# Performance work log

Measured on AMD Instinct MI355X. Metric: run time of the kernel, lower is better.

## Reference

```python
import jax, jax.numpy as jnp
import numpy as np

B, D, LC, LQ = 64, 128, 1024, 128
NEG = -1e30


def setup_inputs() -> dict:
    key = jax.random.key(0)
    k1, k2, k3 = jax.random.split(key, 3)
    lim = float(np.sqrt(1.0 / D))
    return {
        "C": jax.random.normal(k1, (B, D, LC), dtype=jnp.float32),
        "Q": jax.random.normal(k2, (B, D, LQ), dtype=jnp.float32),
        "cmask": jnp.ones((B, LC), dtype=jnp.float32),
        "qmask": jnp.ones((B, LQ), dtype=jnp.float32),
        "w": jax.random.uniform(k3, (3 * D,), dtype=jnp.float32, minval=-lim, maxval=lim),
    }


def reference(C, Q, cmask, qmask, w):
    # C: [B, D, Lc], Q: [B, D, Lq] -> transpose to [B, L, D] as in the torch module
    Ct = jnp.swapaxes(C, 1, 2)  # [B, Lc, D]
    Qt = jnp.swapaxes(Q, 1, 2)  # [B, Lq, D]
    d = Ct.shape[-1]
    # Trilinear decomposition of the per-step concat([Qi, C, Q*C]) . w loop:
    # S[b,c,q] = Qt[b,q] . w_q + Ct[b,c] . w_c + (Ct[b,c] * w_m) . Qt[b,q]
    w_q, w_c, w_m = w[:d], w[d:2 * d], w[2 * d:]
    s_q = Qt @ w_q                                   # [B, Lq]
    s_c = Ct @ w_c                                   # [B, Lc]
    s_m = jnp.einsum("bcd,bqd->bcq", Ct * w_m, Qt)   # [B, Lc, Lq]
    S = s_m + s_c[:, :, None] + s_q[:, None, :]      # [B, Lc, Lq]

    S1 = jax.nn.softmax(S + (1.0 - qmask)[:, None, :] * NEG, axis=2)
    S2 = jax.nn.softmax(S + (1.0 - cmask)[:, :, None] * NEG, axis=1)

    A = jnp.einsum("bcq,bqd->bcd", S1, Qt)           # [B, Lc, D]
    S12 = jnp.einsum("bcq,bkq->bck", S1, S2)         # [B, Lc, Lc]
    Bt = jnp.einsum("bck,bkd->bcd", S12, Ct)         # [B, Lc, D]

    out = jnp.concatenate([Ct, A, Ct * A, Ct * Bt], axis=2)  # [B, Lc, 4D]
    # dropout is identity in eval mode
    return jnp.swapaxes(out, 1, 2)                   # [B, 4D, Lc]
```

## Files before the change

### kernel.cpp

```cpp
#include <hip/hip_runtime.h>
#include <cstdint>
#include <cstddef>

#define B_  64
#define D_  128
#define LC_ 1024
#define LQ_ 128
#define NEGV (-1e30f)
#define NINF (-3.402823466e38f)

typedef short s16x8 __attribute__((ext_vector_type(8)));
typedef float f32x4 __attribute__((ext_vector_type(4)));

__device__ __forceinline__ unsigned short f2bf(float x) {
    union { float f; unsigned u; } v; v.f = x;
    unsigned r = v.u + 0x7fffu + ((v.u >> 16) & 1u);
    return (unsigned short)(r >> 16);
}
__device__ __forceinline__ float bf2f(unsigned short x) {
    union { unsigned u; float f; } v; v.u = ((unsigned)x) << 16;
    return v.f;
}

__global__ __launch_bounds__(256) void kT_C(const float* __restrict__ C,
                                            const float* __restrict__ w,
                                            unsigned short* __restrict__ CWt,
                                            unsigned short* __restrict__ Cb,
                                            float* __restrict__ sc_g) {
    __shared__ float tile[32][33];
    __shared__ float wc_l[128], wm_l[128];
    __shared__ float red[8][32];
    int t = threadIdx.x;
    int b = blockIdx.y, c0 = blockIdx.x * 32;
    if (t < 128) { wc_l[t] = w[D_ + t]; wm_l[t] = w[2 * D_ + t]; }
    __syncthreads();
    float scp = 0.f;
    int cc = t & 31, db = t >> 5;
    for (int ch = 0; ch < 4; ch++) {
#pragma unroll
        for (int i = 0; i < 4; i++) {
            int dl = db * 4 + i;
            float v = C[((size_t)(b * D_ + ch * 32 + dl)) * LC_ + c0 + cc];
            tile[dl][cc] = v;
            scp += v * wc_l[ch * 32 + dl];
        }
        __syncthreads();
        {
            int c2 = t >> 3, ds = (t & 7) * 4;
            ushort4 o;
            o.x = f2bf(tile[ds + 0][c2] * wm_l[ch * 32 + ds + 0]);
            o.y = f2bf(tile[ds + 1][c2] * wm_l[ch * 32 + ds + 1]);
            o.z = f2bf(tile[ds + 2][c2] * wm_l[ch * 32 + ds + 2]);
            o.w = f2bf(tile[ds + 3][c2] * wm_l[ch * 32 + ds + 3]);
            *(ushort4*)&CWt[((size_t)(b * LC_ + c0 + c2)) * D_ + ch * 32 + ds] = o;
        }
        {
            int d2 = t >> 3, cs = (t & 7) * 4;
            ushort4 o;
            o.x = f2bf(tile[d2][cs + 0]);
            o.y = f2bf(tile[d2][cs + 1]);
            o.z = f2bf(tile[d2][cs + 2]);
            o.w = f2bf(tile[d2][cs + 3]);
            *(ushort4*)&Cb[((size_t)(b * D_ + ch * 32 + d2)) * LC_ + c0 + cs] = o;
        }
        __syncthreads();
    }
    red[db][cc] = scp;
    __syncthreads();
    if (t < 32) {
        float s = 0.f;
#pragma unroll
        for (int j = 0; j < 8; j++) s += red[j][t];
        sc_g[b * LC_ + c0 + t] = s;
    }
}

__global__ __launch_bounds__(256) void kT_Q(const float* __restrict__ Q,
                                            const float* __restrict__ w,
                                            unsigned short* __restrict__ Qt,
                                            unsigned short* __restrict__ Qb,
                                            float* __restrict__ sq_g) {
    __shared__ float tile[32][33];
    __shared__ float wq_l[128];
    __shared__ float red[8][32];
    int t = threadIdx.x;
    int b = blockIdx.y, q0 = blockIdx.x * 32;
    if (t < 128) wq_l[t] = w[t];
    __syncthreads();
    float sqp = 0.f;
    int qq = t & 31, db = t >> 5;
    for (int ch = 0; ch < 4; ch++) {
#pragma unroll
        for (int i = 0; i < 4; i++) {
            int dl = db * 4 + i;
            float v = Q[((size_t)(b * D_ + ch * 32 + dl)) * LQ_ + q0 + qq];
            tile[dl][qq] = v;
            sqp += v * wq_l[ch * 32 + dl];
        }
        __syncthreads();
        {
            int q2 = t >> 3, ds = (t & 7) * 4;
            ushort4 o;
            o.x = f2bf(tile[ds + 0][q2]);
            o.y = f2bf(tile[ds + 1][q2]);
            o.z = f2bf(tile[ds + 2][q2]);
            o.w = f2bf(tile[ds + 3][q2]);
            *(ushort4*)&Qt[((size_t)(b * LQ_ + q0 + q2)) * D_ + ch * 32 + ds] = o;
        }
        {
            int d2 = t >> 3, qs = (t & 7) * 4;
            ushort4 o;
            o.x = f2bf(tile[d2][qs + 0]);
            o.y = f2bf(tile[d2][qs + 1]);
            o.z = f2bf(tile[d2][qs + 2]);
            o.w = f2bf(tile[d2][qs + 3]);
            *(ushort4*)&Qb[((size_t)(b * D_ + ch * 32 + d2)) * LQ_ + q0 + qs] = o;
        }
        __syncthreads();
    }
    red[db][qq] = sqp;
    __syncthreads();
    if (t < 32) {
        float s = 0.f;
#pragma unroll
        for (int j = 0; j < 8; j++) s += red[j][t];
        sq_g[b * LQ_ + q0 + t] = s;
    }
}

__global__ __launch_bounds__(256) void kA_S(const unsigned short* __restrict__ CWt,
                                            const unsigned short* __restrict__ Qt,
                                            const float* __restrict__ sc_g,
                                            const float* __restrict__ sq_g,
                                            const float* __restrict__ cmask,
                                            const float* __restrict__ qmask,
                                            unsigned short* __restrict__ S1b,
                                            float* __restrict__ g_g,
                                            float* __restrict__ pmax_g,
                                            float* __restrict__ psum_g) {
    __shared__ unsigned short S1t[128 * 136];
    __shared__ float sc_l[128], sq_l[128], cmv_l[128], qmv_l[128];
    int t = threadIdx.x;
    int b = blockIdx.y, c0 = blockIdx.x * 128;
    if (t < 128) {
        sc_l[t] = sc_g[b * LC_ + c0 + t];
        sq_l[t] = sq_g[b * LQ_ + t];
        cmv_l[t] = (1.0f - cmask[b * LC_ + c0 + t]) * NEGV;
        qmv_l[t] = (1.0f - qmask[b * LQ_ + t]) * NEGV;
    }
    __syncthreads();
    int wv = t >> 6, l = t & 63, quad = l >> 4, lp = l & 15;
    int w32 = wv * 32;
    f32x4 zero = {0.f, 0.f, 0.f, 0.f};
    f32x4 acc[2][8];
#pragma unroll
    for (int mc = 0; mc < 2; mc++)
#pragma unroll
        for (int qt = 0; qt < 8; qt++) acc[mc][qt] = zero;

#pragma unroll
    for (int ks = 0; ks < 4; ks++) {
        s16x8 a[2], bb[8];
        a[0] = *(const s16x8*)&CWt[((size_t)(b * LC_ + c0 + w32 + lp)) * D_ + ks * 32 + quad * 8];
        a[1] = *(const s16x8*)&CWt[((size_t)(b * LC_ + c0 + w32 + 16 + lp)) * D_ + ks * 32 + quad * 8];
#pragma unroll
        for (int qt = 0; qt < 8; qt++)
            bb[qt] = *(const s16x8*)&Qt[((size_t)(b * LQ_ + qt * 16 + lp)) * D_ + ks * 32 + quad * 8];
#pragma unroll
        for (int mc = 0; mc < 2; mc++)
#pragma unroll
            for (int qt = 0; qt < 8; qt++)
                acc[mc][qt] = __builtin_amdgcn_mfma_f32_16x16x32_bf16(a[mc], bb[qt], acc[mc][qt], 0, 0, 0);
    }
#pragma unroll
    for (int mc = 0; mc < 2; mc++)
#pragma unroll
        for (int qt = 0; qt < 8; qt++)
#pragma unroll
            for (int i = 0; i < 4; i++)
                acc[mc][qt][i] += sc_l[w32 + mc * 16 + quad * 4 + i] + sq_l[qt * 16 + lp];

    float qmv_r[8];
#pragma unroll
    for (int qt = 0; qt < 8; qt++) qmv_r[qt] = qmv_l[qt * 16 + lp];

    float rm_r[2][4], ri_r[2][4];
#pragma unroll
    for (int mc = 0; mc < 2; mc++)
#pragma unroll
        for (int i = 0; i < 4; i++) {
            float m = NINF;
#pragma unroll
            for (int qt = 0; qt < 8; qt++) m = fmaxf(m, acc[mc][qt][i] + qmv_r[qt]);
#pragma unroll
            for (int off = 1; off < 16; off <<= 1) m = fmaxf(m, __shfl_xor(m, off, 64));
            float s = 0.f;
#pragma unroll
            for (int qt = 0; qt < 8; qt++) s += __expf(acc[mc][qt][i] + qmv_r[qt] - m);
#pragma unroll
            for (int off = 1; off < 16; off <<= 1) s += __shfl_xor(s, off, 64);
            rm_r[mc][i] = m;
            ri_r[mc][i] = 1.0f / s;
            int row = w32 + mc * 16 + quad * 4 + i;
            if (lp == 0) g_g[b * LC_ + c0 + row] = s * __expf(m + cmv_l[row]);
        }

    float cmv_r[2][4];
#pragma unroll
    for (int mc = 0; mc < 2; mc++)
#pragma unroll
        for (int i = 0; i < 4; i++) cmv_r[mc][i] = cmv_l[w32 + mc * 16 + quad * 4 + i];
    int chunk = blockIdx.x * 4 + wv;
#pragma unroll
    for (int qt = 0; qt < 8; qt++) {
        float cm = NINF;
#pragma unroll
        for (int mc = 0; mc < 2; mc++)
#pragma unroll
            for (int i = 0; i < 4; i++) cm = fmaxf(cm, acc[mc][qt][i] + cmv_r[mc][i]);
        cm = fmaxf(cm, __shfl_xor(cm, 16, 64));
        cm = fmaxf(cm, __shfl_xor(cm, 32, 64));
        float cs = 0.f;
#pragma unroll
        for (int mc = 0; mc < 2; mc++)
#pragma unroll
            for (int i = 0; i < 4; i++) cs += __expf(acc[mc][qt][i] + cmv_r[mc][i] - cm);
        cs += __shfl_xor(cs, 16, 64);
        cs += __shfl_xor(cs, 32, 64);
        if (l < 16) {
            pmax_g[((size_t)(b * 32 + chunk)) * LQ_ + qt * 16 + lp] = cm;
            psum_g[((size_t)(b * 32 + chunk)) * LQ_ + qt * 16 + lp] = cs;
        }
    }

#pragma unroll
    for (int mc = 0; mc < 2; mc++)
#pragma unroll
        for (int qt = 0; qt < 8; qt++)
#pragma unroll
            for (int i = 0; i < 4; i++) {
                int row = w32 + mc * 16 + quad * 4 + i;
                float s1 = __expf(acc[mc][qt][i] + qmv_r[qt] - rm_r[mc][i]) * ri_r[mc][i];
                S1t[row * 136 + qt * 16 + lp] = f2bf(s1);
            }
    __syncthreads();
    {
        int row = t >> 1, qh = (t & 1) * 64;
        const uint4* src = (const uint4*)&S1t[row * 136 + qh];
        uint4* dst = (uint4*)&S1b[((size_t)(b * LC_ + c0 + row)) * LQ_ + qh];
#pragma unroll
        for (int j = 0; j < 8; j++) dst[j] = src[j];
    }
}

__global__ __launch_bounds__(128) void k2b(const float* __restrict__ pmax,
                                           const float* __restrict__ psum,
                                           float* __restrict__ hq_g,
                                           float* __restrict__ ci_g) {
    int q = threadIdx.x, b = blockIdx.x;
    float m = NINF;
    for (int j = 0; j < 32; j++) m = fmaxf(m, pmax[((size_t)(b * 32 + j)) * LQ_ + q]);
    float s = 0.f;
    for (int j = 0; j < 32; j++)
        s += psum[((size_t)(b * 32 + j)) * LQ_ + q] * __expf(pmax[((size_t)(b * 32 + j)) * LQ_ + q] - m);
    hq_g[b * LQ_ + q] = __expf(-m);
    ci_g[b * LQ_ + q] = 1.0f / s;
}

__global__ __launch_bounds__(256) void kB_T2(const unsigned short* __restrict__ Cb,
                                             const unsigned short* __restrict__ S1b,
                                             const float* __restrict__ g_g,
                                             const float* __restrict__ hq_g,
                                             float* __restrict__ T2p) {
    __shared__ unsigned short Ew[64 * 72];
    __shared__ float h_l[64];
    int t = threadIdx.x;
    int b = blockIdx.y;
    int kc = blockIdx.x >> 1, nq = blockIdx.x & 1;
    int q0 = nq * 64, cbase = kc * 256;
    if (t < 64) h_l[t] = hq_g[b * LQ_ + q0 + t];
    int wv = t >> 6, l = t & 63, quad = l >> 4, lp = l & 15;
    int w32 = wv * 32;
    f32x4 zero = {0.f, 0.f, 0.f, 0.f};
    f32x4 acc[2][4];
#pragma unroll
    for (int mc = 0; mc < 2; mc++)
#pragma unroll
        for (int nt = 0; nt < 4; nt++) acc[mc][nt] = zero;
    __syncthreads();

    for (int sub = 0; sub < 4; sub++) {
        int csub = cbase + sub * 64;
#pragma unroll
        for (int r = 0; r < 2; r++) {
            int cr = (t >> 3) + 32 * r;
            int qof = (t & 7) * 8;
            float gv = g_g[b * LC_ + csub + cr];
            uint4 v = *(const uint4*)&S1b[((size_t)(b * LC_ + csub + cr)) * LQ_ + q0 + qof];
            const unsigned short* pu = (const unsigned short*)&v;
#pragma unroll
            for (int j = 0; j < 8; j++)
                Ew[(qof + j) * 72 + cr] = f2bf(bf2f(pu[j]) * gv * h_l[qof + j]);
        }
        __syncthreads();
#pragma unroll
        for (int ks = 0; ks < 2; ks++) {
            s16x8 a[2], bb[4];
            a[0] = *(const s16x8*)&Cb[((size_t)(b * D_ + w32 + lp)) * LC_ + csub + ks * 32 + quad * 8];
            a[1] = *(const s16x8*)&Cb[((size_t)(b * D_ + w32 + 16 + lp)) * LC_ + csub + ks * 32 + quad * 8];
#pragma unroll
            for (int nt = 0; nt < 4; nt++)
                bb[nt] = *(const s16x8*)&Ew[(nt * 16 + lp) * 72 + ks * 32 + quad * 8];
#pragma unroll
            for (int mc = 0; mc < 2; mc++)
#pragma unroll
                for (int nt = 0; nt < 4; nt++)
                    acc[mc][nt] = __builtin_amdgcn_mfma_f32_16x16x32_bf16(a[mc], bb[nt], acc[mc][nt], 0, 0, 0);
        }
        __syncthreads();
    }
#pragma unroll
    for (int mc = 0; mc < 2; mc++)
#pragma unroll
        for (int i = 0; i < 4; i++) {
            int d = w32 + mc * 16 + quad * 4 + i;
#pragma unroll
            for (int nt = 0; nt < 4; nt++)
                T2p[(((size_t)kc * B_ + b) * D_ + d) * LQ_ + q0 + nt * 16 + lp] = acc[mc][nt][i];
        }
}

__global__ __launch_bounds__(256) void k3b(const float* __restrict__ T2p,
                                           const float* __restrict__ ci_g,
                                           unsigned short* __restrict__ T2b) {
    int idx = blockIdx.x * 256 + threadIdx.x;
    const size_t N = (size_t)B_ * D_ * LQ_;
    int b = idx >> 14, q = idx & 127;
    float s = T2p[idx] + T2p[idx + N] + T2p[idx + 2 * N] + T2p[idx + 3 * N];
    T2b[idx] = f2bf(s * ci_g[b * LQ_ + q]);
}

__global__ __launch_bounds__(256) void kC_out(const float* __restrict__ C,
                                              const unsigned short* __restrict__ Qb,
                                              const unsigned short* __restrict__ T2b,
                                              const unsigned short* __restrict__ S1b,
                                              float* __restrict__ out) {
    int t = threadIdx.x;
    int b = blockIdx.y, c0 = blockIdx.x * 128;
    int wv = t >> 6, l = t & 63, quad = l >> 4, lp = l & 15;
    int w32 = wv * 32;
    f32x4 zero = {0.f, 0.f, 0.f, 0.f};
    f32x4 accA[2][8], accB[2][8];
#pragma unroll
    for (int mc = 0; mc < 2; mc++)
#pragma unroll
        for (int nt = 0; nt < 8; nt++) { accA[mc][nt] = zero; accB[mc][nt] = zero; }

#pragma unroll
    for (int ks = 0; ks < 4; ks++) {
        s16x8 aq[2], at[2], bb[8];
        aq[0] = *(const s16x8*)&Qb[((size_t)(b * D_ + w32 + lp)) * LQ_ + ks * 32 + quad * 8];
        aq[1] = *(const s16x8*)&Qb[((size_t)(b * D_ + w32 + 16 + lp)) * LQ_ + ks * 32 + quad * 8];
        at[0] = *(const s16x8*)&T2b[((size_t)(b * D_ + w32 + lp)) * LQ_ + ks * 32 + quad * 8];
        at[1] = *(const s16x8*)&T2b[((size_t)(b * D_ + w32 + 16 + lp)) * LQ_ + ks * 32 + quad * 8];
#pragma unroll
        for (int nt = 0; nt < 8; nt++)
            bb[nt] = *(const s16x8*)&S1b[((size_t)(b * LC_ + c0 + nt * 16 + lp)) * LQ_ + ks * 32 + quad * 8];
#pragma unroll
        for (int mc = 0; mc < 2; mc++)
#pragma unroll
            for (int nt = 0; nt < 8; nt++) {
                accA[mc][nt] = __builtin_amdgcn_mfma_f32_16x16x32_bf16(aq[mc], bb[nt], accA[mc][nt], 0, 0, 0);
                accB[mc][nt] = __builtin_amdgcn_mfma_f32_16x16x32_bf16(at[mc], bb[nt], accB[mc][nt], 0, 0, 0);
            }
    }
    const size_t DL = (size_t)D_ * LC_;
#pragma unroll
    for (int mc = 0; mc < 2; mc++)
#pragma unroll
        for (int i = 0; i < 4; i++) {
            int d = w32 + mc * 16 + quad * 4 + i;
            const float* Crow = C + ((size_t)(b * D_ + d)) * LC_ + c0;
            size_t ob = ((size_t)(b * 4 * D_ + d)) * LC_ + c0;
#pragma unroll
            for (int nt = 0; nt < 8; nt++) {
                int c = nt * 16 + lp;
                float cv = Crow[c];
                float a = accA[mc][nt][i];
                float bt = accB[mc][nt][i];
                out[ob + c] = cv;
                out[ob + DL + c] = a;
                out[ob + 2 * DL + c] = cv * a;
                out[ob + 3 * DL + c] = cv * bt;
            }
        }
}

extern "C" void kernel_launch(void* const* d_in, const int* in_sizes, int n_in,
                              void* d_out, int out_size, void* d_ws, size_t ws_size,
                              hipStream_t stream) {
    const float* C     = (const float*)d_in[0];
    const float* Q     = (const float*)d_in[1];
    const float* cmask = (const float*)d_in[2];
    const float* qmask = (const float*)d_in[3];
    const float* w     = (const float*)d_in[4];
    float* out = (float*)d_out;

    unsigned short* us = (unsigned short*)d_ws;
    unsigned short* S1b = us;
    unsigned short* CWt = S1b + (size_t)B_ * LC_ * LQ_;
    unsigned short* Cb  = CWt + (size_t)B_ * LC_ * D_;
    unsigned short* Qt  = Cb  + (size_t)B_ * D_ * LC_;
    unsigned short* Qb  = Qt  + (size_t)B_ * LQ_ * D_;
    unsigned short* T2b = Qb  + (size_t)B_ * D_ * LQ_;
    float* fp = (float*)(T2b + (size_t)B_ * D_ * LQ_);
    float* T2p    = fp;
    float* sc_g   = T2p + (size_t)4 * B_ * D_ * LQ_;
    float* g_g    = sc_g + (size_t)B_ * LC_;
    float* pmax_g = g_g + (size_t)B_ * LC_;
    float* psum_g = pmax_g + (size_t)B_ * 32 * LQ_;
    float* sq_g   = psum_g + (size_t)B_ * 32 * LQ_;
    float* hq_g   = sq_g + (size_t)B_ * LQ_;
    float* ci_g   = hq_g + (size_t)B_ * LQ_;

    kT_C<<<dim3(LC_ / 32, B_), 256, 0, stream>>>(C, w, CWt, Cb, sc_g);
    kT_Q<<<dim3(LQ_ / 32, B_), 256, 0, stream>>>(Q, w, Qt, Qb, sq_g);
    kA_S<<<dim3(LC_ / 128, B_), 256, 0, stream>>>(CWt, Qt, sc_g, sq_g, cmask, qmask,
                                                  S1b, g_g, pmax_g, psum_g);
    k2b<<<dim3(B_), 128, 0, stream>>>(pmax_g, psum_g, hq_g, ci_g);
    kB_T2<<<dim3(8, B_), 256, 0, stream>>>(Cb, S1b, g_g, hq_g, T2p);
    k3b<<<dim3(B_ * D_ * LQ_ / 256), 256, 0, stream>>>(T2p, ci_g, T2b);
    kC_out<<<dim3(LC_ / 128, B_), 256, 0, stream>>>(C, Qb, T2b, S1b, out);
}
```

Before: 254.8 us.

## Emit pre-scaled transposed S1 from score kernel and stage output writes via LDS

The score kernel now also writes a transposed, g-scaled bf16 copy of S1 (q-major) so the T2 GEMM kernel can load MFMA operands directly from global memory, with no LDS staging, per-element rescaling or barriers. The per-column hq scale moves into the final reduction kernel, and the T2 partial split goes from 4 to 8 chunks. The output kernel transposes accumulators through a swizzled LDS tile so it can write float4-coalesced rows instead of scattered scalar stores. The cost is an extra global S1Et buffer, more partial-sum traffic, and an additional bf16 rounding of the g-scaled S1 before the hq factor is applied.

```diff
diff --git a/kernel.cpp b/kernel.cpp
--- a/kernel.cpp
+++ b/kernel.cpp
@@ -21,6 +21,8 @@
     union { unsigned u; float f; } v; v.u = ((unsigned)x) << 16;
     return v.f;
 }
+
+#define SW(r, c) ((c) ^ (((r) & 7) << 2))
 
 __global__ __launch_bounds__(256) void kT_C(const float* __restrict__ C,
                                             const float* __restrict__ w,
@@ -135,11 +137,11 @@
                                             const float* __restrict__ cmask,
                                             const float* __restrict__ qmask,
                                             unsigned short* __restrict__ S1b,
-                                            float* __restrict__ g_g,
+                                            unsigned short* __restrict__ S1Et,
                                             float* __restrict__ pmax_g,
                                             float* __restrict__ psum_g) {
-    __shared__ unsigned short S1t[128 * 136];
-    __shared__ float sc_l[128], sq_l[128], cmv_l[128], qmv_l[128];
+    __shared__ unsigned short Tt[128 * 136];
+    __shared__ float sc_l[128], sq_l[128], cmv_l[128], qmv_l[128], gs[128];
     int t = threadIdx.x;
     int b = blockIdx.y, c0 = blockIdx.x * 128;
     if (t < 128) {
@@ -202,7 +204,7 @@
             rm_r[mc][i] = m;
             ri_r[mc][i] = 1.0f / s;
             int row = w32 + mc * 16 + quad * 4 + i;
-            if (lp == 0) g_g[b * LC_ + c0 + row] = s * __expf(m + cmv_l[row]);
+            if (lp == 0) gs[row] = s * __expf(m + cmv_l[row]);
         }
 
     float cmv_r[2][4];
@@ -241,15 +243,33 @@
             for (int i = 0; i < 4; i++) {
                 int row = w32 + mc * 16 + quad * 4 + i;
                 float s1 = __expf(acc[mc][qt][i] + qmv_r[qt] - rm_r[mc][i]) * ri_r[mc][i];
-                S1t[row * 136 + qt * 16 + lp] = f2bf(s1);
+                Tt[row * 136 + qt * 16 + lp] = f2bf(s1);
             }
     __syncthreads();
     {
         int row = t >> 1, qh = (t & 1) * 64;
-        const uint4* src = (const uint4*)&S1t[row * 136 + qh];
+        const uint4* src = (const uint4*)&Tt[row * 136 + qh];
         uint4* dst = (uint4*)&S1b[((size_t)(b * LC_ + c0 + row)) * LQ_ + qh];
 #pragma unroll
         for (int j = 0; j < 8; j++) dst[j] = src[j];
+    }
+    {
+        int r4 = t >> 2;
+        int cq = (t & 3) * 8;
+#pragma unroll
+        for (int qh = 0; qh < 2; qh++) {
+            int q = qh * 64 + r4;
+#pragma unroll
+            for (int j = 0; j < 4; j++) {
+                int c = j * 32 + cq;
+                uint4 pk;
+                unsigned short* po = (unsigned short*)&pk;
+#pragma unroll
+                for (int k = 0; k < 8; k++)
+                    po[k] = f2bf(bf2f(Tt[(c + k) * 136 + q]) * gs[c + k]);
+                *(uint4*)&S1Et[((size_t)(b * LQ_ + q)) * LC_ + c0 + c] = pk;
+            }
+        }
     }
 }
 
@@ -268,56 +288,33 @@
 }
 
 __global__ __launch_bounds__(256) void kB_T2(const unsigned short* __restrict__ Cb,
-                                             const unsigned short* __restrict__ S1b,
-                                             const float* __restrict__ g_g,
-                                             const float* __restrict__ hq_g,
+                                             const unsigned short* __restrict__ S1Et,
                                              float* __restrict__ T2p) {
-    __shared__ unsigned short Ew[64 * 72];
-    __shared__ float h_l[64];
     int t = threadIdx.x;
-    int b = blockIdx.y;
-    int kc = blockIdx.x >> 1, nq = blockIdx.x & 1;
-    int q0 = nq * 64, cbase = kc * 256;
-    if (t < 64) h_l[t] = hq_g[b * LQ_ + q0 + t];
+    int b = blockIdx.y, kc = blockIdx.x;
+    int cbase = kc * 128;
     int wv = t >> 6, l = t & 63, quad = l >> 4, lp = l & 15;
     int w32 = wv * 32;
     f32x4 zero = {0.f, 0.f, 0.f, 0.f};
-    f32x4 acc[2][4];
-#pragma unroll
-    for (int mc = 0; mc < 2; mc++)
-#pragma unroll
-        for (int nt = 0; nt < 4; nt++) acc[mc][nt] = zero;
-    __syncthreads();
-
-    for (int sub = 0; sub < 4; sub++) {
-        int csub = cbase + sub * 64;
-#pragma unroll
-        for (int r = 0; r < 2; r++) {
-            int cr = (t >> 3) + 32 * r;
-            int qof = (t & 7) * 8;
-            float gv = g_g[b * LC_ + csub + cr];
-            uint4 v = *(const uint4*)&S1b[((size_t)(b * LC_ + csub + cr)) * LQ_ + q0 + qof];
-            const unsigned short* pu = (const unsigned short*)&v;
-#pragma unroll
-            for (int j = 0; j < 8; j++)
-                Ew[(qof + j) * 72 + cr] = f2bf(bf2f(pu[j]) * gv * h_l[qof + j]);
-        }
-        __syncthreads();
-#pragma unroll
-        for (int ks = 0; ks < 2; ks++) {
-            s16x8 a[2], bb[4];
-            a[0] = *(const s16x8*)&Cb[((size_t)(b * D_ + w32 + lp)) * LC_ + csub + ks * 32 + quad * 8];
-            a[1] = *(const s16x8*)&Cb[((size_t)(b * D_ + w32 + 16 + lp)) * LC_ + csub + ks * 32 + quad * 8];
-#pragma unroll
-            for (int nt = 0; nt < 4; nt++)
-                bb[nt] = *(const s16x8*)&Ew[(nt * 16 + lp) * 72 + ks * 32 + quad * 8];
-#pragma unroll
-            for (int mc = 0; mc < 2; mc++)
-#pragma unroll
-                for (int nt = 0; nt < 4; nt++)
-                    acc[mc][nt] = __builtin_amdgcn_mfma_f32_16x16x32_bf16(a[mc], bb[nt], acc[mc][nt], 0, 0, 0);
-        }
-        __syncthreads();
+    f32x4 acc[2][8];
+#pragma unroll
+    for (int mc = 0; mc < 2; mc++)
+#pragma unroll
+        for (int nt = 0; nt < 8; nt++) acc[mc][nt] = zero;
+
+#pragma unroll
+    for (int ks = 0; ks < 4; ks++) {
+        s16x8 a[2], bb[8];
+        a[0] = *(const s16x8*)&Cb[((size_t)(b * D_ + w32 + lp)) * LC_ + cbase + ks * 32 + quad * 8];
+        a[1] = *(const s16x8*)&Cb[((size_t)(b * D_ + w32 + 16 + lp)) * LC_ + cbase + ks * 32 + quad * 8];
+#pragma unroll
+        for (int nt = 0; nt < 8; nt++)
+            bb[nt] = *(const s16x8*)&S1Et[((size_t)(b * LQ_ + nt * 16 + lp)) * LC_ + cbase + ks * 32 + quad * 8];
+#pragma unroll
+        for (int mc = 0; mc < 2; mc++)
+#pragma unroll
+            for (int nt = 0; nt < 8; nt++)
+                acc[mc][nt] = __builtin_amdgcn_mfma_f32_16x16x32_bf16(a[mc], bb[nt], acc[mc][nt], 0, 0, 0);
     }
 #pragma unroll
     for (int mc = 0; mc < 2; mc++)
@@ -325,19 +322,22 @@
         for (int i = 0; i < 4; i++) {
             int d = w32 + mc * 16 + quad * 4 + i;
 #pragma unroll
-            for (int nt = 0; nt < 4; nt++)
-                T2p[(((size_t)kc * B_ + b) * D_ + d) * LQ_ + q0 + nt * 16 + lp] = acc[mc][nt][i];
+            for (int nt = 0; nt < 8; nt++)
+                T2p[(((size_t)kc * B_ + b) * D_ + d) * LQ_ + nt * 16 + lp] = acc[mc][nt][i];
         }
 }
 
 __global__ __launch_bounds__(256) void k3b(const float* __restrict__ T2p,
+                                           const float* __restrict__ hq_g,
                                            const float* __restrict__ ci_g,
                                            unsigned short* __restrict__ T2b) {
     int idx = blockIdx.x * 256 + threadIdx.x;
     const size_t N = (size_t)B_ * D_ * LQ_;
     int b = idx >> 14, q = idx & 127;
-    float s = T2p[idx] + T2p[idx + N] + T2p[idx + 2 * N] + T2p[idx + 3 * N];
-    T2b[idx] = f2bf(s * ci_g[b * LQ_ + q]);
+    float s = 0.f;
+#pragma unroll
+    for (int j = 0; j < 8; j++) s += T2p[idx + j * N];
+    T2b[idx] = f2bf(s * hq_g[b * LQ_ + q] * ci_g[b * LQ_ + q]);
 }
 
 __global__ __launch_bounds__(256) void kC_out(const float* __restrict__ C,
@@ -345,6 +345,7 @@
                                               const unsigned short* __restrict__ T2b,
                                               const unsigned short* __restrict__ S1b,
                                               float* __restrict__ out) {
+    __shared__ float Tile[64 * 132];
     int t = threadIdx.x;
     int b = blockIdx.y, c0 = blockIdx.x * 128;
     int wv = t >> 6, l = t & 63, quad = l >> 4, lp = l & 15;
@@ -374,26 +375,54 @@
                 accB[mc][nt] = __builtin_amdgcn_mfma_f32_16x16x32_bf16(at[mc], bb[nt], accB[mc][nt], 0, 0, 0);
             }
     }
+
     const size_t DL = (size_t)D_ * LC_;
-#pragma unroll
-    for (int mc = 0; mc < 2; mc++)
-#pragma unroll
-        for (int i = 0; i < 4; i++) {
-            int d = w32 + mc * 16 + quad * 4 + i;
-            const float* Crow = C + ((size_t)(b * D_ + d)) * LC_ + c0;
-            size_t ob = ((size_t)(b * 4 * D_ + d)) * LC_ + c0;
-#pragma unroll
-            for (int nt = 0; nt < 8; nt++) {
-                int c = nt * 16 + lp;
-                float cv = Crow[c];
-                float a = accA[mc][nt][i];
-                float bt = accB[mc][nt][i];
-                out[ob + c] = cv;
-                out[ob + DL + c] = a;
-                out[ob + 2 * DL + c] = cv * a;
-                out[ob + 3 * DL + c] = cv * bt;
+    int r = t >> 2;
+    int rw = wv * 16;
+#pragma unroll
+    for (int mc = 0; mc < 2; mc++) {
+        int d_st = (r >> 4) * 32 + mc * 16 + (r & 15);
+        const float* Crow = C + ((size_t)(b * D_ + d_st)) * LC_ + c0;
+        size_t ob = ((size_t)(b * 4 * D_ + d_st)) * LC_ + c0;
+        __syncthreads();
+#pragma unroll
+        for (int nt = 0; nt < 8; nt++)
+#pragma unroll
+            for (int i = 0; i < 4; i++) {
+                int row = rw + quad * 4 + i;
+                Tile[row * 132 + SW(row, nt * 16 + lp)] = accA[mc][nt][i];
             }
-        }
+        __syncthreads();
+#pragma unroll
+        for (int j = 0; j < 8; j++) {
+            int c = j * 16 + (t & 3) * 4;
+            float4 a4 = *(const float4*)&Tile[r * 132 + SW(r, c)];
+            float4 cv = *(const float4*)&Crow[c];
+            *(float4*)&out[ob + c] = cv;
+            *(float4*)&out[ob + DL + c] = a4;
+            float4 ca;
+            ca.x = cv.x * a4.x; ca.y = cv.y * a4.y; ca.z = cv.z * a4.z; ca.w = cv.w * a4.w;
+            *(float4*)&out[ob + 2 * DL + c] = ca;
+        }
+        __syncthreads();
+#pragma unroll
+        for (int nt = 0; nt < 8; nt++)
+#pragma unroll
+            for (int i = 0; i < 4; i++) {
+                int row = rw + quad * 4 + i;
+                Tile[row * 132 + SW(row, nt * 16 + lp)] = accB[mc][nt][i];
+            }
+        __syncthreads();
+#pragma unroll
+        for (int j = 0; j < 8; j++) {
+            int c = j * 16 + (t & 3) * 4;
+            float4 b4 = *(const float4*)&Tile[r * 132 + SW(r, c)];
+            float4 cv = *(const float4*)&Crow[c];
+            float4 cb;
+            cb.x = cv.x * b4.x; cb.y = cv.y * b4.y; cb.z = cv.z * b4.z; cb.w = cv.w * b4.w;
+            *(float4*)&out[ob + 3 * DL + c] = cb;
+        }
+    }
 }
 
 extern "C" void kernel_launch(void* const* d_in, const int* in_sizes, int n_in,
@@ -407,17 +436,17 @@
     float* out = (float*)d_out;
 
     unsigned short* us = (unsigned short*)d_ws;
-    unsigned short* S1b = us;
-    unsigned short* CWt = S1b + (size_t)B_ * LC_ * LQ_;
-    unsigned short* Cb  = CWt + (size_t)B_ * LC_ * D_;
-    unsigned short* Qt  = Cb  + (size_t)B_ * D_ * LC_;
-    unsigned short* Qb  = Qt  + (size_t)B_ * LQ_ * D_;
-    unsigned short* T2b = Qb  + (size_t)B_ * D_ * LQ_;
+    unsigned short* S1b  = us;
+    unsigned short* S1Et = S1b  + (size_t)B_ * LC_ * LQ_;
+    unsigned short* CWt  = S1Et + (size_t)B_ * LQ_ * LC_;
+    unsigned short* Cb   = CWt  + (size_t)B_ * LC_ * D_;
+    unsigned short* Qt   = Cb   + (size_t)B_ * D_ * LC_;
+    unsigned short* Qb   = Qt   + (size_t)B_ * LQ_ * D_;
+    unsigned short* T2b  = Qb   + (size_t)B_ * D_ * LQ_;
     float* fp = (float*)(T2b + (size_t)B_ * D_ * LQ_);
     float* T2p    = fp;
-    float* sc_g   = T2p + (size_t)4 * B_ * D_ * LQ_;
-    float* g_g    = sc_g + (size_t)B_ * LC_;
-    float* pmax_g = g_g + (size_t)B_ * LC_;
+    float* sc_g   = T2p + (size_t)8 * B_ * D_ * LQ_;
+    float* pmax_g = sc_g + (size_t)B_ * LC_;
     float* psum_g = pmax_g + (size_t)B_ * 32 * LQ_;
     float* sq_g   = psum_g + (size_t)B_ * 32 * LQ_;
     float* hq_g   = sq_g + (size_t)B_ * LQ_;
@@ -426,9 +455,9 @@
     kT_C<<<dim3(LC_ / 32, B_), 256, 0, stream>>>(C, w, CWt, Cb, sc_g);
     kT_Q<<<dim3(LQ_ / 32, B_), 256, 0, stream>>>(Q, w, Qt, Qb, sq_g);
     kA_S<<<dim3(LC_ / 128, B_), 256, 0, stream>>>(CWt, Qt, sc_g, sq_g, cmask, qmask,
-                                                  S1b, g_g, pmax_g, psum_g);
+                                                  S1b, S1Et, pmax_g, psum_g);
     k2b<<<dim3(B_), 128, 0, stream>>>(pmax_g, psum_g, hq_g, ci_g);
-    kB_T2<<<dim3(8, B_), 256, 0, stream>>>(Cb, S1b, g_g, hq_g, T2p);
-    k3b<<<dim3(B_ * D_ * LQ_ / 256), 256, 0, stream>>>(T2p, ci_g, T2b);
+    kB_T2<<<dim3(8, B_), 256, 0, stream>>>(Cb, S1Et, T2p);
+    k3b<<<dim3(B_ * D_ * LQ_ / 256), 256, 0, stream>>>(T2p, hq_g, ci_g, T2b);
     kC_out<<<dim3(LC_ / 128, B_), 256, 0, stream>>>(C, Qb, T2b, S1b, out);
 }
```

Measured after the change: 280.6 us. 10.1% more time.

## Fuse C transpose and T2 partial GEMM into score kernel, drop C staging buffers

Applied to the files above, without the earlier changes.

Removes the separate C transpose/convert kernel and the T2 GEMM kernel. The score kernel now loads C directly, builds the w_m-scaled bf16 tile in LDS, computes s_c on the fly, and right after the softmax computes the per-block partial T2 = C·(S1·g) using an LDS-transposed, g-weighted copy of S1. The hq scaling moves into the reduction kernel, which now sums 8 partials instead of 4. The output kernel is retiled to 64 columns to launch more blocks. This avoids writing and re-reading the CWt/Cb/g intermediates and saves two launches, at the cost of more LDS per block, a longer serial kernel, and twice the partial-sum traffic.

```diff
diff --git a/kernel.cpp b/kernel.cpp
--- a/kernel.cpp
+++ b/kernel.cpp
@@ -17,69 +17,12 @@
     unsigned r = v.u + 0x7fffu + ((v.u >> 16) & 1u);
     return (unsigned short)(r >> 16);
 }
-__device__ __forceinline__ float bf2f(unsigned short x) {
-    union { unsigned u; float f; } v; v.u = ((unsigned)x) << 16;
-    return v.f;
-}
-
-__global__ __launch_bounds__(256) void kT_C(const float* __restrict__ C,
-                                            const float* __restrict__ w,
-                                            unsigned short* __restrict__ CWt,
-                                            unsigned short* __restrict__ Cb,
-                                            float* __restrict__ sc_g) {
-    __shared__ float tile[32][33];
-    __shared__ float wc_l[128], wm_l[128];
-    __shared__ float red[8][32];
-    int t = threadIdx.x;
-    int b = blockIdx.y, c0 = blockIdx.x * 32;
-    if (t < 128) { wc_l[t] = w[D_ + t]; wm_l[t] = w[2 * D_ + t]; }
-    __syncthreads();
-    float scp = 0.f;
-    int cc = t & 31, db = t >> 5;
-    for (int ch = 0; ch < 4; ch++) {
-#pragma unroll
-        for (int i = 0; i < 4; i++) {
-            int dl = db * 4 + i;
-            float v = C[((size_t)(b * D_ + ch * 32 + dl)) * LC_ + c0 + cc];
-            tile[dl][cc] = v;
-            scp += v * wc_l[ch * 32 + dl];
-        }
-        __syncthreads();
-        {
-            int c2 = t >> 3, ds = (t & 7) * 4;
-            ushort4 o;
-            o.x = f2bf(tile[ds + 0][c2] * wm_l[ch * 32 + ds + 0]);
-            o.y = f2bf(tile[ds + 1][c2] * wm_l[ch * 32 + ds + 1]);
-            o.z = f2bf(tile[ds + 2][c2] * wm_l[ch * 32 + ds + 2]);
-            o.w = f2bf(tile[ds + 3][c2] * wm_l[ch * 32 + ds + 3]);
-            *(ushort4*)&CWt[((size_t)(b * LC_ + c0 + c2)) * D_ + ch * 32 + ds] = o;
-        }
-        {
-            int d2 = t >> 3, cs = (t & 7) * 4;
-            ushort4 o;
-            o.x = f2bf(tile[d2][cs + 0]);
-            o.y = f2bf(tile[d2][cs + 1]);
-            o.z = f2bf(tile[d2][cs + 2]);
-            o.w = f2bf(tile[d2][cs + 3]);
-            *(ushort4*)&Cb[((size_t)(b * D_ + ch * 32 + d2)) * LC_ + c0 + cs] = o;
-        }
-        __syncthreads();
-    }
-    red[db][cc] = scp;
-    __syncthreads();
-    if (t < 32) {
-        float s = 0.f;
-#pragma unroll
-        for (int j = 0; j < 8; j++) s += red[j][t];
-        sc_g[b * LC_ + c0 + t] = s;
-    }
-}
-
-__global__ __launch_bounds__(256) void kT_Q(const float* __restrict__ Q,
-                                            const float* __restrict__ w,
-                                            unsigned short* __restrict__ Qt,
-                                            unsigned short* __restrict__ Qb,
-                                            float* __restrict__ sq_g) {
+
+__global__ __launch_bounds__(256) void kQ(const float* __restrict__ Q,
+                                          const float* __restrict__ w,
+                                          unsigned short* __restrict__ Qt,
+                                          unsigned short* __restrict__ Qb,
+                                          float* __restrict__ sq_g) {
     __shared__ float tile[32][33];
     __shared__ float wq_l[128];
     __shared__ float red[8][32];
@@ -128,27 +71,67 @@
     }
 }
 
-__global__ __launch_bounds__(256) void kA_S(const unsigned short* __restrict__ CWt,
-                                            const unsigned short* __restrict__ Qt,
-                                            const float* __restrict__ sc_g,
-                                            const float* __restrict__ sq_g,
-                                            const float* __restrict__ cmask,
-                                            const float* __restrict__ qmask,
-                                            unsigned short* __restrict__ S1b,
-                                            float* __restrict__ g_g,
-                                            float* __restrict__ pmax_g,
-                                            float* __restrict__ psum_g) {
-    __shared__ unsigned short S1t[128 * 136];
-    __shared__ float sc_l[128], sq_l[128], cmv_l[128], qmv_l[128];
+__global__ __launch_bounds__(256) void kS(const float* __restrict__ C,
+                                          const unsigned short* __restrict__ Qt,
+                                          const float* __restrict__ w,
+                                          const float* __restrict__ sq_g,
+                                          const float* __restrict__ cmask,
+                                          const float* __restrict__ qmask,
+                                          unsigned short* __restrict__ S1b,
+                                          float* __restrict__ pmax_g,
+                                          float* __restrict__ psum_g,
+                                          float* __restrict__ T2p) {
+    __shared__ unsigned short CW[128 * 136];
+    __shared__ unsigned short Tg[128 * 136];
+    __shared__ float stage[32][33];
+    __shared__ float wc_l[128], wm_l[128], sq_l[128], cmv_l[128], qmv_l[128], sc_l[128];
+    __shared__ float red[8][32];
+
     int t = threadIdx.x;
     int b = blockIdx.y, c0 = blockIdx.x * 128;
     if (t < 128) {
-        sc_l[t] = sc_g[b * LC_ + c0 + t];
+        wc_l[t] = w[D_ + t];
+        wm_l[t] = w[2 * D_ + t];
         sq_l[t] = sq_g[b * LQ_ + t];
         cmv_l[t] = (1.0f - cmask[b * LC_ + c0 + t]) * NEGV;
         qmv_l[t] = (1.0f - qmask[b * LQ_ + t]) * NEGV;
     }
     __syncthreads();
+
+    int cc = t & 31, db = t >> 5;
+    for (int ch = 0; ch < 4; ch++) {
+        float scp = 0.f;
+        for (int dh = 0; dh < 4; dh++) {
+#pragma unroll
+            for (int i = 0; i < 4; i++) {
+                int dl = db * 4 + i;
+                float v = C[((size_t)(b * D_ + dh * 32 + dl)) * LC_ + c0 + ch * 32 + cc];
+                stage[dl][cc] = v;
+                scp += v * wc_l[dh * 32 + dl];
+            }
+            __syncthreads();
+            {
+                int c2 = t >> 3, ds = (t & 7) * 4;
+                ushort4 o;
+                o.x = f2bf(stage[ds + 0][c2] * wm_l[dh * 32 + ds + 0]);
+                o.y = f2bf(stage[ds + 1][c2] * wm_l[dh * 32 + ds + 1]);
+                o.z = f2bf(stage[ds + 2][c2] * wm_l[dh * 32 + ds + 2]);
+                o.w = f2bf(stage[ds + 3][c2] * wm_l[dh * 32 + ds + 3]);
+                *(ushort4*)&CW[(ch * 32 + c2) * 136 + dh * 32 + ds] = o;
+            }
+            __syncthreads();
+        }
+        red[db][cc] = scp;
+        __syncthreads();
+        if (db == 0) {
+            float s = 0.f;
+#pragma unroll
+            for (int j = 0; j < 8; j++) s += red[j][cc];
+            sc_l[ch * 32 + cc] = s;
+        }
+        __syncthreads();
+    }
+
     int wv = t >> 6, l = t & 63, quad = l >> 4, lp = l & 15;
     int w32 = wv * 32;
     f32x4 zero = {0.f, 0.f, 0.f, 0.f};
@@ -161,8 +144,8 @@
 #pragma unroll
     for (int ks = 0; ks < 4; ks++) {
         s16x8 a[2], bb[8];
-        a[0] = *(const s16x8*)&CWt[((size_t)(b * LC_ + c0 + w32 + lp)) * D_ + ks * 32 + quad * 8];
-        a[1] = *(const s16x8*)&CWt[((size_t)(b * LC_ + c0 + w32 + 16 + lp)) * D_ + ks * 32 + quad * 8];
+        a[0] = *(const s16x8*)&CW[(w32 + lp) * 136 + ks * 32 + quad * 8];
+        a[1] = *(const s16x8*)&CW[(w32 + 16 + lp) * 136 + ks * 32 + quad * 8];
 #pragma unroll
         for (int qt = 0; qt < 8; qt++)
             bb[qt] = *(const s16x8*)&Qt[((size_t)(b * LQ_ + qt * 16 + lp)) * D_ + ks * 32 + quad * 8];
@@ -184,11 +167,12 @@
 #pragma unroll
     for (int qt = 0; qt < 8; qt++) qmv_r[qt] = qmv_l[qt * 16 + lp];
 
-    float rm_r[2][4], ri_r[2][4];
+    float rm_r[2][4], ri_r[2][4], gs_r[2][4];
 #pragma unroll
     for (int mc = 0; mc < 2; mc++)
 #pragma unroll
         for (int i = 0; i < 4; i++) {
+            int row = w32 + mc * 16 + quad * 4 + i;
             float m = NINF;
 #pragma unroll
             for (int qt = 0; qt < 8; qt++) m = fmaxf(m, acc[mc][qt][i] + qmv_r[qt]);
@@ -201,8 +185,7 @@
             for (int off = 1; off < 16; off <<= 1) s += __shfl_xor(s, off, 64);
             rm_r[mc][i] = m;
             ri_r[mc][i] = 1.0f / s;
-            int row = w32 + mc * 16 + quad * 4 + i;
-            if (lp == 0) g_g[b * LC_ + c0 + row] = s * __expf(m + cmv_l[row]);
+            gs_r[mc][i] = s * __expf(m + cmv_l[row]);
         }
 
     float cmv_r[2][4];
@@ -233,6 +216,7 @@
         }
     }
 
+    __syncthreads();
 #pragma unroll
     for (int mc = 0; mc < 2; mc++)
 #pragma unroll
@@ -240,17 +224,57 @@
 #pragma unroll
             for (int i = 0; i < 4; i++) {
                 int row = w32 + mc * 16 + quad * 4 + i;
+                int q = qt * 16 + lp;
                 float s1 = __expf(acc[mc][qt][i] + qmv_r[qt] - rm_r[mc][i]) * ri_r[mc][i];
-                S1t[row * 136 + qt * 16 + lp] = f2bf(s1);
-            }
-    __syncthreads();
+                CW[row * 136 + q] = f2bf(s1);
+                Tg[q * 136 + row] = f2bf(s1 * gs_r[mc][i]);
+            }
+    __syncthreads();
+
     {
         int row = t >> 1, qh = (t & 1) * 64;
-        const uint4* src = (const uint4*)&S1t[row * 136 + qh];
+        const uint4* src = (const uint4*)&CW[row * 136 + qh];
         uint4* dst = (uint4*)&S1b[((size_t)(b * LC_ + c0 + row)) * LQ_ + qh];
 #pragma unroll
         for (int j = 0; j < 8; j++) dst[j] = src[j];
     }
+
+    f32x4 acc2[2][8];
+#pragma unroll
+    for (int mc = 0; mc < 2; mc++)
+#pragma unroll
+        for (int nt = 0; nt < 8; nt++) acc2[mc][nt] = zero;
+#pragma unroll
+    for (int ks = 0; ks < 4; ks++) {
+        s16x8 a2[2], bb[8];
+#pragma unroll
+        for (int m = 0; m < 2; m++) {
+            int d = w32 + m * 16 + lp;
+            const float4* p = (const float4*)&C[((size_t)(b * D_ + d)) * LC_ + c0 + ks * 32 + quad * 8];
+            float4 v0 = p[0], v1 = p[1];
+            unsigned short* pp = (unsigned short*)&a2[m];
+            pp[0] = f2bf(v0.x); pp[1] = f2bf(v0.y); pp[2] = f2bf(v0.z); pp[3] = f2bf(v0.w);
+            pp[4] = f2bf(v1.x); pp[5] = f2bf(v1.y); pp[6] = f2bf(v1.z); pp[7] = f2bf(v1.w);
+        }
+#pragma unroll
+        for (int nt = 0; nt < 8; nt++)
+            bb[nt] = *(const s16x8*)&Tg[(nt * 16 + lp) * 136 + ks * 32 + quad * 8];
+#pragma unroll
+        for (int m = 0; m < 2; m++)
+#pragma unroll
+            for (int nt = 0; nt < 8; nt++)
+                acc2[m][nt] = __builtin_amdgcn_mfma_f32_16x16x32_bf16(a2[m], bb[nt], acc2[m][nt], 0, 0, 0);
+    }
+    size_t base = ((size_t)(blockIdx.x * B_ + b)) * ((size_t)D_ * LQ_);
+#pragma unroll
+    for (int mc = 0; mc < 2; mc++)
+#pragma unroll
+        for (int i = 0; i < 4; i++) {
+            int d = w32 + mc * 16 + quad * 4 + i;
+#pragma unroll
+            for (int nt = 0; nt < 8; nt++)
+                T2p[base + (size_t)d * LQ_ + nt * 16 + lp] = acc2[mc][nt][i];
+        }
 }
 
 __global__ __launch_bounds__(128) void k2b(const float* __restrict__ pmax,
@@ -267,77 +291,17 @@
     ci_g[b * LQ_ + q] = 1.0f / s;
 }
 
-__global__ __launch_bounds__(256) void kB_T2(const unsigned short* __restrict__ Cb,
-                                             const unsigned short* __restrict__ S1b,
-                                             const float* __restrict__ g_g,
-                                             const float* __restrict__ hq_g,
-                                             float* __restrict__ T2p) {
-    __shared__ unsigned short Ew[64 * 72];
-    __shared__ float h_l[64];
-    int t = threadIdx.x;
-    int b = blockIdx.y;
-    int kc = blockIdx.x >> 1, nq = blockIdx.x & 1;
-    int q0 = nq * 64, cbase = kc * 256;
-    if (t < 64) h_l[t] = hq_g[b * LQ_ + q0 + t];
-    int wv = t >> 6, l = t & 63, quad = l >> 4, lp = l & 15;
-    int w32 = wv * 32;
-    f32x4 zero = {0.f, 0.f, 0.f, 0.f};
-    f32x4 acc[2][4];
-#pragma unroll
-    for (int mc = 0; mc < 2; mc++)
-#pragma unroll
-        for (int nt = 0; nt < 4; nt++) acc[mc][nt] = zero;
-    __syncthreads();
-
-    for (int sub = 0; sub < 4; sub++) {
-        int csub = cbase + sub * 64;
-#pragma unroll
-        for (int r = 0; r < 2; r++) {
-            int cr = (t >> 3) + 32 * r;
-            int qof = (t & 7) * 8;
-            float gv = g_g[b * LC_ + csub + cr];
-            uint4 v = *(const uint4*)&S1b[((size_t)(b * LC_ + csub + cr)) * LQ_ + q0 + qof];
-            const unsigned short* pu = (const unsigned short*)&v;
-#pragma unroll
-            for (int j = 0; j < 8; j++)
-                Ew[(qof + j) * 72 + cr] = f2bf(bf2f(pu[j]) * gv * h_l[qof + j]);
-        }
-        __syncthreads();
-#pragma unroll
-        for (int ks = 0; ks < 2; ks++) {
-            s16x8 a[2], bb[4];
-            a[0] = *(const s16x8*)&Cb[((size_t)(b * D_ + w32 + lp)) * LC_ + csub + ks * 32 + quad * 8];
-            a[1] = *(const s16x8*)&Cb[((size_t)(b * D_ + w32 + 16 + lp)) * LC_ + csub + ks * 32 + quad * 8];
-#pragma unroll
-            for (int nt = 0; nt < 4; nt++)
-                bb[nt] = *(const s16x8*)&Ew[(nt * 16 + lp) * 72 + ks * 32 + quad * 8];
-#pragma unroll
-            for (int mc = 0; mc < 2; mc++)
-#pragma unroll
-                for (int nt = 0; nt < 4; nt++)
-                    acc[mc][nt] = __builtin_amdgcn_mfma_f32_16x16x32_bf16(a[mc], bb[nt], acc[mc][nt], 0, 0, 0);
-        }
-        __syncthreads();
-    }
-#pragma unroll
-    for (int mc = 0; mc < 2; mc++)
-#pragma unroll
-        for (int i = 0; i < 4; i++) {
-            int d = w32 + mc * 16 + quad * 4 + i;
-#pragma unroll
-            for (int nt = 0; nt < 4; nt++)
-                T2p[(((size_t)kc * B_ + b) * D_ + d) * LQ_ + q0 + nt * 16 + lp] = acc[mc][nt][i];
-        }
-}
-
 __global__ __launch_bounds__(256) void k3b(const float* __restrict__ T2p,
+                                           const float* __restrict__ hq_g,
                                            const float* __restrict__ ci_g,
                                            unsigned short* __restrict__ T2b) {
     int idx = blockIdx.x * 256 + threadIdx.x;
     const size_t N = (size_t)B_ * D_ * LQ_;
     int b = idx >> 14, q = idx & 127;
-    float s = T2p[idx] + T2p[idx + N] + T2p[idx + 2 * N] + T2p[idx + 3 * N];
-    T2b[idx] = f2bf(s * ci_g[b * LQ_ + q]);
+    float s = 0.f;
+#pragma unroll
+    for (int j = 0; j < 8; j++) s += T2p[(size_t)j * N + idx];
+    T2b[idx] = f2bf(s * hq_g[b * LQ_ + q] * ci_g[b * LQ_ + q]);
 }
 
 __global__ __launch_bounds__(256) void kC_out(const float* __restrict__ C,
@@ -346,30 +310,30 @@
                                               const unsigned short* __restrict__ S1b,
                                               float* __restrict__ out) {
     int t = threadIdx.x;
-    int b = blockIdx.y, c0 = blockIdx.x * 128;
+    int b = blockIdx.y, c0 = blockIdx.x * 64;
     int wv = t >> 6, l = t & 63, quad = l >> 4, lp = l & 15;
     int w32 = wv * 32;
     f32x4 zero = {0.f, 0.f, 0.f, 0.f};
-    f32x4 accA[2][8], accB[2][8];
-#pragma unroll
-    for (int mc = 0; mc < 2; mc++)
-#pragma unroll
-        for (int nt = 0; nt < 8; nt++) { accA[mc][nt] = zero; accB[mc][nt] = zero; }
+    f32x4 accA[2][4], accB[2][4];
+#pragma unroll
+    for (int mc = 0; mc < 2; mc++)
+#pragma unroll
+        for (int nt = 0; nt < 4; nt++) { accA[mc][nt] = zero; accB[mc][nt] = zero; }
 
 #pragma unroll
     for (int ks = 0; ks < 4; ks++) {
-        s16x8 aq[2], at[2], bb[8];
+        s16x8 aq[2], at[2], bb[4];
         aq[0] = *(const s16x8*)&Qb[((size_t)(b * D_ + w32 + lp)) * LQ_ + ks * 32 + quad * 8];
         aq[1] = *(const s16x8*)&Qb[((size_t)(b * D_ + w32 + 16 + lp)) * LQ_ + ks * 32 + quad * 8];
         at[0] = *(const s16x8*)&T2b[((size_t)(b * D_ + w32 + lp)) * LQ_ + ks * 32 + quad * 8];
         at[1] = *(const s16x8*)&T2b[((size_t)(b * D_ + w32 + 16 + lp)) * LQ_ + ks * 32 + quad * 8];
 #pragma unroll
-        for (int nt = 0; nt < 8; nt++)
+        for (int nt = 0; nt < 4; nt++)
             bb[nt] = *(const s16x8*)&S1b[((size_t)(b * LC_ + c0 + nt * 16 + lp)) * LQ_ + ks * 32 + quad * 8];
 #pragma unroll
         for (int mc = 0; mc < 2; mc++)
 #pragma unroll
-            for (int nt = 0; nt < 8; nt++) {
+            for (int nt = 0; nt < 4; nt++) {
                 accA[mc][nt] = __builtin_amdgcn_mfma_f32_16x16x32_bf16(aq[mc], bb[nt], accA[mc][nt], 0, 0, 0);
                 accB[mc][nt] = __builtin_amdgcn_mfma_f32_16x16x32_bf16(at[mc], bb[nt], accB[mc][nt], 0, 0, 0);
             }
@@ -383,7 +347,7 @@
             const float* Crow = C + ((size_t)(b * D_ + d)) * LC_ + c0;
             size_t ob = ((size_t)(b * 4 * D_ + d)) * LC_ + c0;
 #pragma unroll
-            for (int nt = 0; nt < 8; nt++) {
+            for (int nt = 0; nt < 4; nt++) {
                 int c = nt * 16 + lp;
                 float cv = Crow[c];
                 float a = accA[mc][nt][i];
@@ -408,27 +372,21 @@
 
     unsigned short* us = (unsigned short*)d_ws;
     unsigned short* S1b = us;
-    unsigned short* CWt = S1b + (size_t)B_ * LC_ * LQ_;
-    unsigned short* Cb  = CWt + (size_t)B_ * LC_ * D_;
-    unsigned short* Qt  = Cb  + (size_t)B_ * D_ * LC_;
+    unsigned short* Qt  = S1b + (size_t)B_ * LC_ * LQ_;
     unsigned short* Qb  = Qt  + (size_t)B_ * LQ_ * D_;
     unsigned short* T2b = Qb  + (size_t)B_ * D_ * LQ_;
     float* fp = (float*)(T2b + (size_t)B_ * D_ * LQ_);
     float* T2p    = fp;
-    float* sc_g   = T2p + (size_t)4 * B_ * D_ * LQ_;
-    float* g_g    = sc_g + (size_t)B_ * LC_;
-    float* pmax_g = g_g + (size_t)B_ * LC_;
+    float* pmax_g = T2p + (size_t)8 * B_ * D_ * LQ_;
     float* psum_g = pmax_g + (size_t)B_ * 32 * LQ_;
     float* sq_g   = psum_g + (size_t)B_ * 32 * LQ_;
     float* hq_g   = sq_g + (size_t)B_ * LQ_;
     float* ci_g   = hq_g + (size_t)B_ * LQ_;
 
-    kT_C<<<dim3(LC_ / 32, B_), 256, 0, stream>>>(C, w, CWt, Cb, sc_g);
-    kT_Q<<<dim3(LQ_ / 32, B_), 256, 0, stream>>>(Q, w, Qt, Qb, sq_g);
-    kA_S<<<dim3(LC_ / 128, B_), 256, 0, stream>>>(CWt, Qt, sc_g, sq_g, cmask, qmask,
-                                                  S1b, g_g, pmax_g, psum_g);
+    kQ<<<dim3(LQ_ / 32, B_), 256, 0, stream>>>(Q, w, Qt, Qb, sq_g);
+    kS<<<dim3(LC_ / 128, B_), 256, 0, stream>>>(C, Qt, w, sq_g, cmask, qmask,
+                                                S1b, pmax_g, psum_g, T2p);
     k2b<<<dim3(B_), 128, 0, stream>>>(pmax_g, psum_g, hq_g, ci_g);
-    kB_T2<<<dim3(8, B_), 256, 0, stream>>>(Cb, S1b, g_g, hq_g, T2p);
-    k3b<<<dim3(B_ * D_ * LQ_ / 256), 256, 0, stream>>>(T2p, ci_g, T2b);
-    kC_out<<<dim3(LC_ / 128, B_), 256, 0, stream>>>(C, Qb, T2b, S1b, out);
-}
+    k3b<<<dim3(B_ * D_ * LQ_ / 256), 256, 0, stream>>>(T2p, hq_g, ci_g, T2b);
+    kC_out<<<dim3(LC_ / 64, B_), 256, 0, stream>>>(C, Qb, T2b, S1b, out);
+}
```

Result: faster. 239.6 us (-6.0%).
